# Kernel optimization log

Hardware: AMD Instinct MI355X
Metric: run time of the kernel (lower is better)

Reference implementation:

```python
import jax, jax.numpy as jnp
import numpy as np

B, S, D, H = 64, 64, 4096, 64  # NOTE: code requires S == H (see notes)
HD = D // H  # 64


def setup_inputs() -> dict:
    key = jax.random.key(0)
    ks = jax.random.split(key, 9)
    std = 0.02
    return {
        "x": jax.random.normal(ks[0], (B, S, D), dtype=jnp.float32),
        "Wq": jax.random.normal(ks[1], (D, D), dtype=jnp.float32) * std,
        "bq": jax.random.normal(ks[2], (D,), dtype=jnp.float32) * std,
        "Wk": jax.random.normal(ks[3], (D, D), dtype=jnp.float32) * std,
        "bk": jax.random.normal(ks[4], (D,), dtype=jnp.float32) * std,
        "Wv": jax.random.normal(ks[5], (D, D), dtype=jnp.float32) * std,
        "bv": jax.random.normal(ks[6], (D,), dtype=jnp.float32) * std,
        "Wp": jax.random.normal(ks[7], (D, D), dtype=jnp.float32) * std,
        "bp": jax.random.normal(ks[8], (D,), dtype=jnp.float32) * std,
    }


def reference(x, Wq, bq, Wk, bk, Wv, bv, Wp, bp):
    b, s, d = x.shape
    h, hd = H, d // H
    # q, k: [B,S,D] -> [B,S,H,hd] -> [B,H,S,hd]
    q = (x @ Wq.T + bq).reshape(b, s, h, hd).transpose(0, 2, 1, 3)
    k = (x @ Wk.T + bk).reshape(b, s, h, hd).transpose(0, 2, 1, 3)
    # v: faithfully replicates the original buggy view(B, H, S, hd).transpose(1,2)
    # -> shape [B, S, H, hd] (NOT head-major)
    v = (x @ Wv.T + bv).reshape(b, h, s, hd).transpose(0, 2, 1, 3)
    # attention WITHOUT 1/sqrt(hd) scaling (faithful to source)
    attn = jax.nn.softmax(jnp.einsum("bhqd,bhkd->bhqk", q, k), axis=-1)  # [B,H,S,S]
    # dropout layers are identity in eval mode
    # ShardedTensor: chunk v along last dim into 2 shards of hd/2
    v0, v1 = jnp.split(v, 2, axis=-1)  # each [B,S,H,hd/2]; broadcast needs S==H
    out0 = jnp.matmul(attn, v0)  # [B,H,S,hd/2]
    out1 = jnp.matmul(attn, v1)
    out = jnp.concatenate([out0, out1], axis=0)  # [2B,H,S,hd/2] (faithful cat on dim 0)
    out = out.transpose(0, 2, 1, 3).reshape(b, s, d)  # row-major regroup, same as torch view
    return out @ Wp.T + bp
```

## Files before the change

kernel.cpp:

```cpp
#include <hip/hip_runtime.h>
#include <stdint.h>

typedef __bf16   bf16x8 __attribute__((ext_vector_type(8)));
typedef float    f32x4  __attribute__((ext_vector_type(4)));
typedef uint16_t u16x8  __attribute__((ext_vector_type(8)));

using as1_cvp = const __attribute__((address_space(1))) void*;
using as3_vp  = __attribute__((address_space(3))) void*;

__device__ __forceinline__ uint16_t f2bf(float f) {
    uint32_t u = __float_as_uint(f);
    u += 0x7FFF + ((u >> 16) & 1);
    return (uint16_t)(u >> 16);
}

__device__ __forceinline__ void gload16(const void* g, void* l) {
    __builtin_amdgcn_global_load_lds((as1_cvp)g, (as3_vp)l, 16, 0, 0);
}

#define MFMA16(a, b, c) __builtin_amdgcn_mfma_f32_16x16x32_bf16((a), (b), (c), 0, 0, 0)

__global__ __launch_bounds__(256)
void cvt_bf16(const float* __restrict__ in, uint16_t* __restrict__ out, int n8)
{
    int i = blockIdx.x * 256 + threadIdx.x;
    if (i >= n8) return;
    const float4* p = reinterpret_cast<const float4*>(in) + (size_t)i * 2;
    float4 a = p[0], b = p[1];
    u16x8 o;
    o[0] = f2bf(a.x); o[1] = f2bf(a.y); o[2] = f2bf(a.z); o[3] = f2bf(a.w);
    o[4] = f2bf(b.x); o[5] = f2bf(b.y); o[6] = f2bf(b.z); o[7] = f2bf(b.w);
    reinterpret_cast<u16x8*>(out)[i] = o;
}

template <int OUT_BF16>
__global__ __launch_bounds__(512, 2)
void gemm256(const uint16_t* __restrict__ A, const uint16_t* __restrict__ Bt,
             const float* __restrict__ bias, void* __restrict__ Cout,
             int M, int N, int K)
{
    __shared__ uint16_t lds[65536];
    const int NT = K >> 6;

    int bid = blockIdx.x;
    bid = (bid & 7) * 32 + (bid >> 3);
    const int bx = bid & 15, by = bid >> 4;
    const int rb = by * 256, cb = bx * 256;

    const int tid  = threadIdx.x;
    const int w    = tid >> 6;
    const int lane = tid & 63;
    const int g    = lane >> 4;
    const int l16  = lane & 15;
    const int wm   = w >> 2;
    const int wn   = w & 3;
    const int srow = lane >> 2;
    const int sblk = lane & 3;

    f32x4 acc[8][4] = {};

    auto stageA = [&](int buf, int kh, int kbase) {
#pragma unroll
        for (int i = 0; i < 2; ++i) {
            const int row = i * 128 + w * 16 + srow;
            const uint16_t* src = A + (size_t)(rb + row) * K + kbase
                                    + ((sblk ^ ((row >> 1) & 3)) << 3);
            gload16(src, &lds[(buf * 2 + kh) * 16384 + i * 4096 + w * 512]);
        }
    };
    auto stageB = [&](int buf, int kh, int kbase) {
#pragma unroll
        for (int i = 0; i < 2; ++i) {
            const int row = i * 128 + w * 16 + srow;
            const uint16_t* src = Bt + (size_t)(cb + row) * K + kbase
                                     + ((sblk ^ ((row >> 1) & 3)) << 3);
            gload16(src, &lds[(buf * 2 + kh) * 16384 + 8192 + i * 4096 + w * 512]);
        }
    };

    stageA(0, 0, 0);  stageB(0, 0, 0);
    stageA(0, 1, 32); stageB(0, 1, 32);
    stageA(1, 0, 64); stageB(1, 0, 64);
    asm volatile("s_waitcnt vmcnt(4)" ::: "memory");
    __builtin_amdgcn_s_barrier();

    for (int t = 0; t < NT; ++t) {
        const int cur = t & 1, nxt = cur ^ 1;
        bf16x8 bfr[4];
#pragma unroll
        for (int ph = 0; ph < 4; ++ph) {
            const int kh  = ph >> 1;
            const int grp = ph & 1;
            const int base = (cur * 2 + kh) * 16384;

            bf16x8 af[4];
#pragma unroll
            for (int mi = 0; mi < 4; ++mi) {
                const int r = wm * 128 + grp * 64 + mi * 16 + l16;
                af[mi] = *reinterpret_cast<const bf16x8*>(
                    &lds[base + r * 32 + ((g ^ ((r >> 1) & 3)) << 3)]);
            }
            if (grp == 0) {
#pragma unroll
                for (int n = 0; n < 4; ++n) {
                    const int c = wn * 64 + n * 16 + l16;
                    bfr[n] = *reinterpret_cast<const bf16x8*>(
                        &lds[base + 8192 + c * 32 + ((g ^ ((c >> 1) & 3)) << 3)]);
                }
            }

            if (ph == 0 && t + 1 < NT) stageA(nxt, 1, (t + 1) * 64 + 32);
            if (ph == 1 && t + 1 < NT) stageB(nxt, 1, (t + 1) * 64 + 32);
            if (ph == 2 && t + 2 < NT) stageA(cur, 0, (t + 2) * 64);
            if (ph == 3 && t + 2 < NT) stageB(cur, 0, (t + 2) * 64);

            __builtin_amdgcn_s_barrier();
            asm volatile("s_waitcnt lgkmcnt(0)" ::: "memory");
            __builtin_amdgcn_sched_barrier(0);
            __builtin_amdgcn_s_setprio(1);
#pragma unroll
            for (int mi = 0; mi < 4; ++mi)
#pragma unroll
                for (int n = 0; n < 4; ++n)
                    acc[grp * 4 + mi][n] = MFMA16(af[mi], bfr[n], acc[grp * 4 + mi][n]);
            __builtin_amdgcn_s_setprio(0);
            if (ph == 3) {
                if (t >= NT - 2) asm volatile("s_waitcnt vmcnt(0)" ::: "memory");
                else             asm volatile("s_waitcnt vmcnt(4)" ::: "memory");
            }
            __builtin_amdgcn_s_barrier();
        }
    }

    float bv[4];
#pragma unroll
    for (int n = 0; n < 4; ++n) bv[n] = bias[cb + wn * 64 + n * 16 + l16];

#pragma unroll
    for (int m = 0; m < 8; ++m) {
#pragma unroll
        for (int n = 0; n < 4; ++n) {
            const int col = cb + wn * 64 + n * 16 + l16;
#pragma unroll
            for (int r = 0; r < 4; ++r) {
                const int row = rb + wm * 128 + m * 16 + g * 4 + r;
                float v = acc[m][n][r] + bv[n];
                if (OUT_BF16)
                    ((uint16_t*)Cout)[(size_t)row * N + col] = f2bf(v);
                else
                    ((float*)Cout)[(size_t)row * N + col] = v;
            }
        }
    }
}

__global__ __launch_bounds__(256)
void attn_kernel(const uint16_t* __restrict__ Q, const uint16_t* __restrict__ Kg,
                 const uint16_t* __restrict__ V, uint16_t* __restrict__ Y)
{
    const int bid = blockIdx.x;
    const int hh  = bid & 63;
    const int bb  = bid >> 6;
    const int tid = threadIdx.x;
    const int w   = tid >> 6, lane = tid & 63, g = lane >> 4, l16 = lane & 15;

    __shared__ uint16_t Vt[64 * 64];
    __shared__ uint16_t Pl[64 * 64];

    {
        const int k  = tid >> 2;
        const int l0 = (tid & 3) * 16;
        const uint16_t* src = V + (size_t)(bb * 64 + k) * 4096 + hh * 64 + l0;
        u16x8 v0 = *reinterpret_cast<const u16x8*>(src);
        u16x8 v1 = *reinterpret_cast<const u16x8*>(src + 8);
#pragma unroll
        for (int i = 0; i < 8; ++i) {
            int l = l0 + i;
            Vt[l * 64 + (k ^ ((l & 7) << 3))] = v0[i];
        }
#pragma unroll
        for (int i = 0; i < 8; ++i) {
            int l = l0 + 8 + i;
            Vt[l * 64 + (k ^ ((l & 7) << 3))] = v1[i];
        }
    }

    f32x4 sa[4] = {};
    {
        const uint16_t* qrow = Q + (size_t)(bb * 64 + w * 16 + l16) * 4096 + hh * 64 + g * 8;
        bf16x8 a0 = *reinterpret_cast<const bf16x8*>(qrow);
        bf16x8 a1 = *reinterpret_cast<const bf16x8*>(qrow + 32);
#pragma unroll
        for (int n = 0; n < 4; ++n) {
            const uint16_t* krow = Kg + (size_t)(bb * 64 + n * 16 + l16) * 4096 + hh * 64 + g * 8;
            bf16x8 b0 = *reinterpret_cast<const bf16x8*>(krow);
            bf16x8 b1 = *reinterpret_cast<const bf16x8*>(krow + 32);
            sa[n] = MFMA16(a0, b0, sa[n]);
            sa[n] = MFMA16(a1, b1, sa[n]);
        }
    }

    float p[4][4];
#pragma unroll
    for (int j = 0; j < 4; ++j) {
        float mx = fmaxf(fmaxf(sa[0][j], sa[1][j]), fmaxf(sa[2][j], sa[3][j]));
        mx = fmaxf(mx, __shfl_xor(mx, 1));
        mx = fmaxf(mx, __shfl_xor(mx, 2));
        mx = fmaxf(mx, __shfl_xor(mx, 4));
        mx = fmaxf(mx, __shfl_xor(mx, 8));
        float s = 0.f;
#pragma unroll
        for (int n = 0; n < 4; ++n) { p[n][j] = __expf(sa[n][j] - mx); s += p[n][j]; }
        s += __shfl_xor(s, 1);
        s += __shfl_xor(s, 2);
        s += __shfl_xor(s, 4);
        s += __shfl_xor(s, 8);
        float inv = 1.0f / s;
#pragma unroll
        for (int n = 0; n < 4; ++n) p[n][j] *= inv;
    }

#pragma unroll
    for (int j = 0; j < 4; ++j) {
        const int q = w * 16 + g * 4 + j;
#pragma unroll
        for (int n = 0; n < 4; ++n) {
            const int kcol = n * 16 + l16;
            Pl[q * 64 + (kcol ^ ((q & 7) << 3))] = f2bf(p[n][j]);
        }
    }
    __syncthreads();

    f32x4 oa[4] = {};
    {
        const int qr = w * 16 + l16;
        bf16x8 a0 = *reinterpret_cast<const bf16x8*>(&Pl[qr * 64 + ((g * 8)      ^ ((qr & 7) << 3))]);
        bf16x8 a1 = *reinterpret_cast<const bf16x8*>(&Pl[qr * 64 + ((32 + g * 8) ^ ((qr & 7) << 3))]);
#pragma unroll
        for (int n = 0; n < 4; ++n) {
            const int vr = n * 16 + l16;
            bf16x8 b0 = *reinterpret_cast<const bf16x8*>(&Vt[vr * 64 + ((g * 8)      ^ ((vr & 7) << 3))]);
            bf16x8 b1 = *reinterpret_cast<const bf16x8*>(&Vt[vr * 64 + ((32 + g * 8) ^ ((vr & 7) << 3))]);
            oa[n] = MFMA16(a0, b0, oa[n]);
            oa[n] = MFMA16(a1, b1, oa[n]);
        }
    }

#pragma unroll
    for (int n = 0; n < 4; ++n) {
        const int ll = n * 16 + l16;
#pragma unroll
        for (int r = 0; r < 4; ++r) {
            const int qq = w * 16 + g * 4 + r;
            const int b_ = (bb >> 1) + ((ll >= 32) ? 32 : 0);
            const int s_ = ((bb & 1) << 5) + (qq >> 1);
            const int h_ = ((qq & 1) << 5) + (hh >> 1);
            const int l_ = ((hh & 1) << 5) + (ll & 31);
            Y[(size_t)(b_ * 64 + s_) * 4096 + h_ * 64 + l_] = f2bf(oa[n][r]);
        }
    }
}

extern "C" void kernel_launch(void* const* d_in, const int* in_sizes, int n_in,
                              void* d_out, int out_size, void* d_ws, size_t ws_size,
                              hipStream_t stream)
{
    (void)in_sizes; (void)n_in; (void)out_size; (void)ws_size;

    const float* x  = (const float*)d_in[0];
    const float* Wq = (const float*)d_in[1];
    const float* bq = (const float*)d_in[2];
    const float* Wk = (const float*)d_in[3];
    const float* bk = (const float*)d_in[4];
    const float* Wv = (const float*)d_in[5];
    const float* bv = (const float*)d_in[6];
    const float* Wp = (const float*)d_in[7];
    const float* bp = (const float*)d_in[8];
    float* out = (float*)d_out;

    const size_t NN = 16777216;
    uint16_t* xb   = (uint16_t*)d_ws;
    uint16_t* wb   = xb + NN;
    uint16_t* Qb   = wb + NN;
    uint16_t* Kb   = Qb + NN;
    uint16_t* Vb   = Kb + NN;
    uint16_t* Yb   = xb;

    const int n8 = (int)(NN / 8);
    dim3 cgrid((n8 + 255) / 256), cblk(256);
    dim3 ggrid(256), gblk(512);

    cvt_bf16<<<cgrid, cblk, 0, stream>>>(x, xb, n8);

    cvt_bf16<<<cgrid, cblk, 0, stream>>>(Wq, wb, n8);
    gemm256<1><<<ggrid, gblk, 0, stream>>>(xb, wb, bq, (void*)Qb, 4096, 4096, 4096);

    cvt_bf16<<<cgrid, cblk, 0, stream>>>(Wk, wb, n8);
    gemm256<1><<<ggrid, gblk, 0, stream>>>(xb, wb, bk, (void*)Kb, 4096, 4096, 4096);

    cvt_bf16<<<cgrid, cblk, 0, stream>>>(Wv, wb, n8);
    gemm256<1><<<ggrid, gblk, 0, stream>>>(xb, wb, bv, (void*)Vb, 4096, 4096, 4096);

    attn_kernel<<<dim3(4096), dim3(256), 0, stream>>>(Qb, Kb, Vb, Yb);

    cvt_bf16<<<cgrid, cblk, 0, stream>>>(Wp, wb, n8);
    gemm256<0><<<ggrid, gblk, 0, stream>>>(Yb, wb, bp, (void*)out, 4096, 4096, 4096);
}
```

Measured before the change: 627.9 us.

## Switch GEMM to 32x32x16 MFMA and restructure K-loop into two half-tile phases

Replaces the 16x16x32 bf16 MFMA tiles in the 256x256 GEMM with 32x32x16 MFMAs, so each wave holds a 4x2 grid of 32x32 accumulators and reads fewer, larger LDS fragments per FLOP. The per-iteration schedule moves from four barriered phases to two: it loads both K-halves' fragments up front and then issues all MFMAs, with fewer barriers per K-step. The epilogue is rewritten for the 32x32 output register layout. In exchange, more fragment registers are live at once, and the MFMA work no longer interleaves as tightly with LDS reads and global prefetches.

```diff
diff --git a/kernel.cpp b/kernel.cpp
--- a/kernel.cpp
+++ b/kernel.cpp
@@ -1,9 +1,10 @@
 #include <hip/hip_runtime.h>
 #include <stdint.h>
 
-typedef __bf16   bf16x8 __attribute__((ext_vector_type(8)));
-typedef float    f32x4  __attribute__((ext_vector_type(4)));
-typedef uint16_t u16x8  __attribute__((ext_vector_type(8)));
+typedef __bf16   bf16x8  __attribute__((ext_vector_type(8)));
+typedef float    f32x4   __attribute__((ext_vector_type(4)));
+typedef float    f32x16  __attribute__((ext_vector_type(16)));
+typedef uint16_t u16x8   __attribute__((ext_vector_type(8)));
 
 using as1_cvp = const __attribute__((address_space(1))) void*;
 using as3_vp  = __attribute__((address_space(3))) void*;
@@ -19,6 +20,7 @@
 }
 
 #define MFMA16(a, b, c) __builtin_amdgcn_mfma_f32_16x16x32_bf16((a), (b), (c), 0, 0, 0)
+#define MFMA32(a, b, c) __builtin_amdgcn_mfma_f32_32x32x16_bf16((a), (b), (c), 0, 0, 0)
 
 __global__ __launch_bounds__(256)
 void cvt_bf16(const float* __restrict__ in, uint16_t* __restrict__ out, int n8)
@@ -50,14 +52,14 @@
     const int tid  = threadIdx.x;
     const int w    = tid >> 6;
     const int lane = tid & 63;
-    const int g    = lane >> 4;
-    const int l16  = lane & 15;
+    const int l32  = lane & 31;
+    const int l5   = lane >> 5;
     const int wm   = w >> 2;
     const int wn   = w & 3;
     const int srow = lane >> 2;
     const int sblk = lane & 3;
 
-    f32x4 acc[8][4] = {};
+    f32x16 acc[4][2] = {};
 
     auto stageA = [&](int buf, int kh, int kbase) {
 #pragma unroll
@@ -78,6 +80,17 @@
         }
     };
 
+    auto readA = [&](int base, int mi, int ks) -> bf16x8 {
+        const int r = wm * 128 + mi * 32 + l32;
+        return *reinterpret_cast<const bf16x8*>(
+            &lds[base + r * 32 + (((ks * 2 + l5) ^ ((r >> 1) & 3)) << 3)]);
+    };
+    auto readB = [&](int base, int ni, int ks) -> bf16x8 {
+        const int c = wn * 64 + ni * 32 + l32;
+        return *reinterpret_cast<const bf16x8*>(
+            &lds[base + 8192 + c * 32 + (((ks * 2 + l5) ^ ((c >> 1) & 3)) << 3)]);
+    };
+
     stageA(0, 0, 0);  stageB(0, 0, 0);
     stageA(0, 1, 32); stageB(0, 1, 32);
     stageA(1, 0, 64); stageB(1, 0, 64);
@@ -86,65 +99,73 @@
 
     for (int t = 0; t < NT; ++t) {
         const int cur = t & 1, nxt = cur ^ 1;
-        bf16x8 bfr[4];
-#pragma unroll
-        for (int ph = 0; ph < 4; ++ph) {
-            const int kh  = ph >> 1;
-            const int grp = ph & 1;
-            const int base = (cur * 2 + kh) * 16384;
-
-            bf16x8 af[4];
-#pragma unroll
-            for (int mi = 0; mi < 4; ++mi) {
-                const int r = wm * 128 + grp * 64 + mi * 16 + l16;
-                af[mi] = *reinterpret_cast<const bf16x8*>(
-                    &lds[base + r * 32 + ((g ^ ((r >> 1) & 3)) << 3)]);
-            }
-            if (grp == 0) {
-#pragma unroll
-                for (int n = 0; n < 4; ++n) {
-                    const int c = wn * 64 + n * 16 + l16;
-                    bfr[n] = *reinterpret_cast<const bf16x8*>(
-                        &lds[base + 8192 + c * 32 + ((g ^ ((c >> 1) & 3)) << 3)]);
-                }
-            }
-
-            if (ph == 0 && t + 1 < NT) stageA(nxt, 1, (t + 1) * 64 + 32);
-            if (ph == 1 && t + 1 < NT) stageB(nxt, 1, (t + 1) * 64 + 32);
-            if (ph == 2 && t + 2 < NT) stageA(cur, 0, (t + 2) * 64);
-            if (ph == 3 && t + 2 < NT) stageB(cur, 0, (t + 2) * 64);
-
-            __builtin_amdgcn_s_barrier();
-            asm volatile("s_waitcnt lgkmcnt(0)" ::: "memory");
-            __builtin_amdgcn_sched_barrier(0);
-            __builtin_amdgcn_s_setprio(1);
+        const int base0 = (cur * 2 + 0) * 16384;
+        const int base1 = (cur * 2 + 1) * 16384;
+
+        if (t + 1 < NT) { stageA(nxt, 1, (t + 1) * 64 + 32);
+                          stageB(nxt, 1, (t + 1) * 64 + 32); }
+        bf16x8 a0[4][2], b0[2][2];
+#pragma unroll
+        for (int mi = 0; mi < 4; ++mi)
+#pragma unroll
+            for (int ks = 0; ks < 2; ++ks) a0[mi][ks] = readA(base0, mi, ks);
+#pragma unroll
+        for (int ni = 0; ni < 2; ++ni)
+#pragma unroll
+            for (int ks = 0; ks < 2; ++ks) b0[ni][ks] = readB(base0, ni, ks);
+
+        __builtin_amdgcn_sched_barrier(0);
+        __builtin_amdgcn_s_barrier();
+
+        if (t + 2 < NT) { stageA(cur, 0, (t + 2) * 64);
+                          stageB(cur, 0, (t + 2) * 64); }
+        bf16x8 a1[4][2], b1[2][2];
+#pragma unroll
+        for (int mi = 0; mi < 4; ++mi)
+#pragma unroll
+            for (int ks = 0; ks < 2; ++ks) a1[mi][ks] = readA(base1, mi, ks);
+#pragma unroll
+        for (int ni = 0; ni < 2; ++ni)
+#pragma unroll
+            for (int ks = 0; ks < 2; ++ks) b1[ni][ks] = readB(base1, ni, ks);
+
+        __builtin_amdgcn_s_setprio(1);
+#pragma unroll
+        for (int ks = 0; ks < 2; ++ks)
 #pragma unroll
             for (int mi = 0; mi < 4; ++mi)
 #pragma unroll
-                for (int n = 0; n < 4; ++n)
-                    acc[grp * 4 + mi][n] = MFMA16(af[mi], bfr[n], acc[grp * 4 + mi][n]);
-            __builtin_amdgcn_s_setprio(0);
-            if (ph == 3) {
-                if (t >= NT - 2) asm volatile("s_waitcnt vmcnt(0)" ::: "memory");
-                else             asm volatile("s_waitcnt vmcnt(4)" ::: "memory");
-            }
-            __builtin_amdgcn_s_barrier();
-        }
-    }
-
-    float bv[4];
-#pragma unroll
-    for (int n = 0; n < 4; ++n) bv[n] = bias[cb + wn * 64 + n * 16 + l16];
-
-#pragma unroll
-    for (int m = 0; m < 8; ++m) {
-#pragma unroll
-        for (int n = 0; n < 4; ++n) {
-            const int col = cb + wn * 64 + n * 16 + l16;
-#pragma unroll
-            for (int r = 0; r < 4; ++r) {
-                const int row = rb + wm * 128 + m * 16 + g * 4 + r;
-                float v = acc[m][n][r] + bv[n];
+                for (int ni = 0; ni < 2; ++ni)
+                    acc[mi][ni] = MFMA32(a0[mi][ks], b0[ni][ks], acc[mi][ni]);
+#pragma unroll
+        for (int ks = 0; ks < 2; ++ks)
+#pragma unroll
+            for (int mi = 0; mi < 4; ++mi)
+#pragma unroll
+                for (int ni = 0; ni < 2; ++ni)
+                    acc[mi][ni] = MFMA32(a1[mi][ks], b1[ni][ks], acc[mi][ni]);
+        __builtin_amdgcn_s_setprio(0);
+
+        __builtin_amdgcn_sched_barrier(0);
+        if (t >= NT - 2) asm volatile("s_waitcnt vmcnt(0)" ::: "memory");
+        else             asm volatile("s_waitcnt vmcnt(4)" ::: "memory");
+        __builtin_amdgcn_s_barrier();
+    }
+
+    float bv[2];
+#pragma unroll
+    for (int ni = 0; ni < 2; ++ni) bv[ni] = bias[cb + wn * 64 + ni * 32 + l32];
+
+#pragma unroll
+    for (int mi = 0; mi < 4; ++mi) {
+#pragma unroll
+        for (int ni = 0; ni < 2; ++ni) {
+            const int col = cb + wn * 64 + ni * 32 + l32;
+#pragma unroll
+            for (int reg = 0; reg < 16; ++reg) {
+                const int row = rb + wm * 128 + mi * 32
+                              + (reg & 3) + 8 * (reg >> 2) + 4 * l5;
+                float v = acc[mi][ni][reg] + bv[ni];
                 if (OUT_BF16)
                     ((uint16_t*)Cout)[(size_t)row * N + col] = f2bf(v);
                 else
```

Result: slower. 666.3 us (+6.1%).

## Software-pipeline LDS fragment reads ahead of MFMAs in the GEMM main loop

Applied to the files above, without the earlier changes.

Reorganizes each K-iteration of the bf16 GEMM into four explicit stages, each loading the next stage's A/B fragments from LDS before issuing the current stage's MFMA group. This replaces the old per-phase pattern of barrier, full lgkmcnt drain, then MFMA with one barrier per stage, and lets LDS reads overlap matrix math. The cost is more live fragment registers, which may raise register pressure. It also relies on the barrier placement to keep the buffer-reuse ordering safe for the prefetch writes.

```diff
diff --git a/kernel.cpp b/kernel.cpp
--- a/kernel.cpp
+++ b/kernel.cpp
@@ -1,9 +1,9 @@
 #include <hip/hip_runtime.h>
 #include <stdint.h>
 
-typedef __bf16   bf16x8 __attribute__((ext_vector_type(8)));
-typedef float    f32x4  __attribute__((ext_vector_type(4)));
-typedef uint16_t u16x8  __attribute__((ext_vector_type(8)));
+typedef __bf16   bf16x8  __attribute__((ext_vector_type(8)));
+typedef float    f32x4   __attribute__((ext_vector_type(4)));
+typedef uint16_t u16x8   __attribute__((ext_vector_type(8)));
 
 using as1_cvp = const __attribute__((address_space(1))) void*;
 using as3_vp  = __attribute__((address_space(3))) void*;
@@ -78,6 +78,33 @@
         }
     };
 
+    auto readA = [&](int base, int grp, bf16x8* dst) {
+#pragma unroll
+        for (int mi = 0; mi < 4; ++mi) {
+            const int r = wm * 128 + grp * 64 + mi * 16 + l16;
+            dst[mi] = *reinterpret_cast<const bf16x8*>(
+                &lds[base + r * 32 + ((g ^ ((r >> 1) & 3)) << 3)]);
+        }
+    };
+    auto readB = [&](int base, bf16x8* dst) {
+#pragma unroll
+        for (int n = 0; n < 4; ++n) {
+            const int c = wn * 64 + n * 16 + l16;
+            dst[n] = *reinterpret_cast<const bf16x8*>(
+                &lds[base + 8192 + c * 32 + ((g ^ ((c >> 1) & 3)) << 3)]);
+        }
+    };
+
+    auto mfma_grp = [&](int grp, const bf16x8* af, const bf16x8* bf) {
+        __builtin_amdgcn_s_setprio(1);
+#pragma unroll
+        for (int mi = 0; mi < 4; ++mi)
+#pragma unroll
+            for (int n = 0; n < 4; ++n)
+                acc[grp * 4 + mi][n] = MFMA16(af[mi], bf[n], acc[grp * 4 + mi][n]);
+        __builtin_amdgcn_s_setprio(0);
+    };
+
     stageA(0, 0, 0);  stageB(0, 0, 0);
     stageA(0, 1, 32); stageB(0, 1, 32);
     stageA(1, 0, 64); stageB(1, 0, 64);
@@ -86,50 +113,36 @@
 
     for (int t = 0; t < NT; ++t) {
         const int cur = t & 1, nxt = cur ^ 1;
-        bf16x8 bfr[4];
-#pragma unroll
-        for (int ph = 0; ph < 4; ++ph) {
-            const int kh  = ph >> 1;
-            const int grp = ph & 1;
-            const int base = (cur * 2 + kh) * 16384;
-
-            bf16x8 af[4];
-#pragma unroll
-            for (int mi = 0; mi < 4; ++mi) {
-                const int r = wm * 128 + grp * 64 + mi * 16 + l16;
-                af[mi] = *reinterpret_cast<const bf16x8*>(
-                    &lds[base + r * 32 + ((g ^ ((r >> 1) & 3)) << 3)]);
-            }
-            if (grp == 0) {
-#pragma unroll
-                for (int n = 0; n < 4; ++n) {
-                    const int c = wn * 64 + n * 16 + l16;
-                    bfr[n] = *reinterpret_cast<const bf16x8*>(
-                        &lds[base + 8192 + c * 32 + ((g ^ ((c >> 1) & 3)) << 3)]);
-                }
-            }
-
-            if (ph == 0 && t + 1 < NT) stageA(nxt, 1, (t + 1) * 64 + 32);
-            if (ph == 1 && t + 1 < NT) stageB(nxt, 1, (t + 1) * 64 + 32);
-            if (ph == 2 && t + 2 < NT) stageA(cur, 0, (t + 2) * 64);
-            if (ph == 3 && t + 2 < NT) stageB(cur, 0, (t + 2) * 64);
-
-            __builtin_amdgcn_s_barrier();
-            asm volatile("s_waitcnt lgkmcnt(0)" ::: "memory");
-            __builtin_amdgcn_sched_barrier(0);
-            __builtin_amdgcn_s_setprio(1);
-#pragma unroll
-            for (int mi = 0; mi < 4; ++mi)
-#pragma unroll
-                for (int n = 0; n < 4; ++n)
-                    acc[grp * 4 + mi][n] = MFMA16(af[mi], bfr[n], acc[grp * 4 + mi][n]);
-            __builtin_amdgcn_s_setprio(0);
-            if (ph == 3) {
-                if (t >= NT - 2) asm volatile("s_waitcnt vmcnt(0)" ::: "memory");
-                else             asm volatile("s_waitcnt vmcnt(4)" ::: "memory");
-            }
-            __builtin_amdgcn_s_barrier();
-        }
+        const int b0 = (cur * 2 + 0) * 16384;
+        const int b1 = (cur * 2 + 1) * 16384;
+        bf16x8 af0[4], af1[4], af2[4], af3[4], bf0[4], bf1[4];
+
+        if (t + 1 < NT) stageA(nxt, 1, (t + 1) * 64 + 32);
+        readA(b0, 0, af0); readB(b0, bf0);
+        readA(b0, 1, af1);
+        mfma_grp(0, af0, bf0);
+        __builtin_amdgcn_sched_barrier(0);
+        __builtin_amdgcn_s_barrier();
+
+        if (t + 1 < NT) stageB(nxt, 1, (t + 1) * 64 + 32);
+        readB(b1, bf1);
+        readA(b1, 0, af2);
+        mfma_grp(1, af1, bf0);
+        __builtin_amdgcn_sched_barrier(0);
+        __builtin_amdgcn_s_barrier();
+
+        if (t + 2 < NT) stageA(cur, 0, (t + 2) * 64);
+        readA(b1, 1, af3);
+        mfma_grp(0, af2, bf1);
+        __builtin_amdgcn_sched_barrier(0);
+        __builtin_amdgcn_s_barrier();
+
+        if (t + 2 < NT) stageB(cur, 0, (t + 2) * 64);
+        mfma_grp(1, af3, bf1);
+        __builtin_amdgcn_sched_barrier(0);
+        if (t >= NT - 2) asm volatile("s_waitcnt vmcnt(0)" ::: "memory");
+        else             asm volatile("s_waitcnt vmcnt(4)" ::: "memory");
+        __builtin_amdgcn_s_barrier();
     }
 
     float bv[4];
```

Measured after the change: 598.9 us. -4.6%, faster.
